# Kernel optimization log

Hardware: AMD Instinct MI355X
Metric: run time of the kernel (lower is better)

Reference implementation:

```python
import jax, jax.numpy as jnp
import numpy as np

B, N, E = 4, 50000, 800000
C_IN, C_OUT, OUT = 64, 64, 32


def _uniform(key, shape, fan_in):
    s = 1.0 / np.sqrt(fan_in)
    return jax.random.uniform(key, shape, jnp.float32, -s, s)


def setup_inputs() -> dict:
    key = jax.random.key(0)
    ks = jax.random.split(key, 16)
    x = jax.random.normal(ks[0], (B, N, C_IN), jnp.float32)
    edge_index = jax.random.randint(ks[1], (2, E), 0, N, jnp.int64)
    edge_weight = jax.random.uniform(ks[2], (E,), jnp.float32)
    # GCNConv weights (in->out) and biases for z, r, h gates
    Wz = _uniform(ks[3], (C_IN, C_OUT), C_IN); bz = jnp.zeros((C_OUT,), jnp.float32)
    Wr = _uniform(ks[4], (C_IN, C_OUT), C_IN); br = jnp.zeros((C_OUT,), jnp.float32)
    Wh = _uniform(ks[5], (C_IN, C_OUT), C_IN); bh = jnp.zeros((C_OUT,), jnp.float32)
    # gating Linears: (2*out -> out)
    Lz = _uniform(ks[6], (2 * C_OUT, C_OUT), 2 * C_OUT); Lzb = _uniform(ks[7], (C_OUT,), 2 * C_OUT)
    Lr = _uniform(ks[8], (2 * C_OUT, C_OUT), 2 * C_OUT); Lrb = _uniform(ks[9], (C_OUT,), 2 * C_OUT)
    Lh = _uniform(ks[10], (2 * C_OUT, C_OUT), 2 * C_OUT); Lhb = _uniform(ks[11], (C_OUT,), 2 * C_OUT)
    # output head Linear(out_channels -> out_size)
    Hw = _uniform(ks[12], (C_OUT, OUT), C_OUT); Hb = _uniform(ks[13], (OUT,), C_OUT)
    return dict(x=x, edge_index=edge_index, edge_weight=edge_weight,
                Wz=Wz, bz=bz, Wr=Wr, br=br, Wh=Wh, bh=bh,
                Lz=Lz, Lzb=Lzb, Lr=Lr, Lrb=Lrb, Lh=Lh, Lhb=Lhb,
                Hw=Hw, Hb=Hb)


def _gcn(x, W, b, src, tgt, norm):
    # x: (B, N, Cin) -> (B, N, Cout); sym-normalized aggregation over edges
    xw = jnp.einsum('bnf,fo->bno', x, W)
    msg = xw[:, src] * norm[None, :, None]          # (B, E+N, Cout)
    agg = jnp.zeros_like(xw).at[:, tgt].add(msg)    # scatter-add at targets
    return agg + b


def reference(x, edge_index, edge_weight, Wz, bz, Wr, br, Wh, bh,
              Lz, Lzb, Lr, Lrb, Lh, Lhb, Hw, Hb):
    src, tgt = edge_index[0], edge_index[1]
    loop = jnp.arange(N)
    src_f = jnp.concatenate([src, loop])
    tgt_f = jnp.concatenate([tgt, loop])
    w_f = jnp.concatenate([edge_weight, jnp.ones((N,), edge_weight.dtype)])
    deg = jnp.zeros((N,), w_f.dtype).at[tgt_f].add(w_f)  # self-loops => deg >= 1
    dinv = jax.lax.rsqrt(deg)
    norm = dinv[src_f] * w_f * dinv[tgt_f]
    H = jnp.zeros((x.shape[0], N, Wz.shape[1]), x.dtype)  # TGCN2 initial hidden state
    gz = _gcn(x, Wz, bz, src_f, tgt_f, norm)
    Z = jax.nn.sigmoid(jnp.concatenate([gz, H], -1) @ Lz + Lzb)
    gr = _gcn(x, Wr, br, src_f, tgt_f, norm)
    R = jax.nn.sigmoid(jnp.concatenate([gr, H], -1) @ Lr + Lrb)
    gh = _gcn(x, Wh, bh, src_f, tgt_f, norm)
    Ht = jnp.tanh(jnp.concatenate([gh, H * R], -1) @ Lh + Lhb)
    Hn = Z * H + (1.0 - Z) * Ht
    return jax.nn.relu(Hn) @ Hw + Hb
```

## Files before the change

### kernel.cpp

```cpp
#include <hip/hip_runtime.h>
#include <stdint.h>

#define N_NODES 50000
#define N_EDGES 800000
#define XSTRIDE 3200000
#define PS      3200000
#define PSU     1600000
#define EBLK    3125
#define XPBLK   12500
#define MAXDEG  64
#define CSH     24
#define WMASK   0xFFFFFFu

typedef __attribute__((ext_vector_type(8))) short short8;
typedef __attribute__((ext_vector_type(4))) float float4v;

static __device__ __forceinline__ unsigned f2bf(float f) {
  unsigned u = __float_as_uint(f);
  return (u + 0x7fffu + ((u >> 16) & 1u)) >> 16;
}
static __device__ __forceinline__ float bflo(unsigned u) { return __uint_as_float(u << 16); }
static __device__ __forceinline__ float bfhi(unsigned u) { return __uint_as_float(u & 0xffff0000u); }

__global__ __launch_bounds__(256) void k_atomic_frag(
    const int* __restrict__ tgt, const int* __restrict__ src,
    const float* __restrict__ ew,
    unsigned* __restrict__ packed32, int2* __restrict__ colw,
    const float* __restrict__ Wz, const float* __restrict__ bz,
    const float* __restrict__ Wh, const float* __restrict__ bh,
    const float* __restrict__ Lz, const float* __restrict__ Lzb,
    const float* __restrict__ Lh, const float* __restrict__ Lhb,
    const float* __restrict__ Hw,
    ushort* __restrict__ BG, ushort* __restrict__ BH, float* __restrict__ czh) {
  int blk = blockIdx.x;
  if (blk < EBLK) {
    int e = blk * 256 + threadIdx.x;
    int t = tgt[e], s = src[e];
    t = t < 0 ? 0 : (t >= N_NODES ? N_NODES - 1 : t);
    s = s < 0 ? 0 : (s >= N_NODES ? N_NODES - 1 : s);
    float wv = ew[e];
    wv = wv < 0.f ? 0.f : wv;
    unsigned fix = (unsigned)(wv * 262144.0f);
    fix = fix > 262143u ? 262143u : fix;
    unsigned old = atomicAdd(&packed32[t], (1u << CSH) | fix);
    unsigned rank = old >> CSH;
    if (rank < MAXDEG)
      colw[t * MAXDEG + (int)rank] = make_int2(s, __float_as_int(wv));
    return;
  }
  int idx = (blk - EBLK) * 256 + threadIdx.x;
  if (idx < 16384) {
    int i = idx & 7, lane = (idx >> 3) & 63, kk = (idx >> 9) & 1;
    int jt = (idx >> 10) & 7, hilo = idx >> 13;
    int c = kk * 32 + ((lane >> 4) << 3) + i;
    int jj0 = jt * 16 + (lane & 15);
    const float* W = (jj0 < 64) ? Wz : Wh;
    const float* L = (jj0 < 64) ? Lz : Lh;
    int jj = jj0 & 63;
    float v = 0.f;
    #pragma unroll 8
    for (int k = 0; k < 64; ++k) v += W[c * 64 + k] * L[k * 64 + jj];
    unsigned hi = f2bf(v);
    BG[idx] = hilo ? (ushort)f2bf(v - bflo(hi)) : (ushort)hi;
  } else if (idx < 20480) {
    int t = idx - 16384;
    int i = t & 7, lane = (t >> 3) & 63, kk = (t >> 9) & 1;
    int ot = (t >> 10) & 1, hilo = (t >> 11) & 1;
    int c = kk * 32 + ((lane >> 4) << 3) + i;
    int o = ot * 16 + (lane & 15);
    float v = Hw[c * 32 + o];
    unsigned hi = f2bf(v);
    BH[t] = hilo ? (ushort)f2bf(v - bflo(hi)) : (ushort)hi;
  } else if (idx < 20608) {
    int jj0 = idx - 20480;
    int jj = jj0 & 63;
    const float* L  = (jj0 < 64) ? Lz  : Lh;
    const float* bb = (jj0 < 64) ? bz  : bh;
    const float* Lb = (jj0 < 64) ? Lzb : Lhb;
    float v = Lb[jj];
    #pragma unroll 8
    for (int k = 0; k < 64; ++k) v += bb[k] * L[k * 64 + jj];
    czh[jj0] = v;
  }
}

__global__ __launch_bounds__(256) void k_xpose(
    const float* __restrict__ x, const unsigned* __restrict__ packed32,
    uint2* __restrict__ xp) {
  int i = blockIdx.x * 256 + threadIdx.x;
  int n = i >> 6;
  unsigned pk = packed32[n];
  float dinv = rsqrtf(1.0f + (float)(pk & WMASK) * 0x1p-18f);
  float v0 = x[i] * dinv;
  float v1 = x[i + XSTRIDE] * dinv;
  float v2 = x[i + 2 * XSTRIDE] * dinv;
  float v3 = x[i + 3 * XSTRIDE] * dinv;
  uint2 u;
  u.x = (f2bf(v1) << 16) | f2bf(v0);
  u.y = (f2bf(v3) << 16) | f2bf(v2);
  xp[i] = u;
}

__global__ __launch_bounds__(256) void kagg(
    const uint4* __restrict__ xp4, const unsigned* __restrict__ packed32,
    const int4* __restrict__ colw4, unsigned* __restrict__ aggp32) {
  int lane = threadIdx.x & 63;
  int w = threadIdx.x >> 6;
  int n = blockIdx.x * 4 + w;
  int c2 = lane & 31;
  int eh = lane >> 5;
  unsigned pk = packed32[n];
  int cnt = (int)(pk >> CSH);
  cnt = cnt > MAXDEG ? MAXDEG : cnt;
  float dinv_n = rsqrtf(1.0f + (float)(pk & WMASK) * 0x1p-18f);
  float a0, a1, a2, a3, b0, b1, b2, b3;
  {
    float g = eh ? 0.0f : 1.0f;
    uint4 q = xp4[(size_t)n * 32 + c2];
    a0 = g * bflo(q.x); a1 = g * bfhi(q.x);
    a2 = g * bflo(q.y); a3 = g * bfhi(q.y);
    b0 = g * bflo(q.z); b1 = g * bfhi(q.z);
    b2 = g * bflo(q.w); b3 = g * bfhi(q.w);
  }
  const int4* row = colw4 + (size_t)n * (MAXDEG / 2);
  const int2* row2 = (const int2*)row;
  int p = 0;
  for (; p + 8 <= cnt; p += 8) {
    int4 m0 = row[(p >> 1) + 2 * eh];
    int4 m1 = row[(p >> 1) + 2 * eh + 1];
    float w0 = __int_as_float(m0.y), w1 = __int_as_float(m0.w);
    float w2 = __int_as_float(m1.y), w3 = __int_as_float(m1.w);
    uint4 q0 = xp4[(size_t)m0.x * 32 + c2];
    uint4 q1 = xp4[(size_t)m0.z * 32 + c2];
    uint4 q2 = xp4[(size_t)m1.x * 32 + c2];
    uint4 q3 = xp4[(size_t)m1.z * 32 + c2];
    a0 += w0*bflo(q0.x) + w1*bflo(q1.x) + w2*bflo(q2.x) + w3*bflo(q3.x);
    a1 += w0*bfhi(q0.x) + w1*bfhi(q1.x) + w2*bfhi(q2.x) + w3*bfhi(q3.x);
    a2 += w0*bflo(q0.y) + w1*bflo(q1.y) + w2*bflo(q2.y) + w3*bflo(q3.y);
    a3 += w0*bfhi(q0.y) + w1*bfhi(q1.y) + w2*bfhi(q2.y) + w3*bfhi(q3.y);
    b0 += w0*bflo(q0.z) + w1*bflo(q1.z) + w2*bflo(q2.z) + w3*bflo(q3.z);
    b1 += w0*bfhi(q0.z) + w1*bfhi(q1.z) + w2*bfhi(q2.z) + w3*bfhi(q3.z);
    b2 += w0*bflo(q0.w) + w1*bflo(q1.w) + w2*bflo(q2.w) + w3*bflo(q3.w);
    b3 += w0*bfhi(q0.w) + w1*bfhi(q1.w) + w2*bfhi(q2.w) + w3*bfhi(q3.w);
  }
  for (; p + 2 <= cnt; p += 2) {
    int2 m = row2[p + eh];
    float wv = __int_as_float(m.y);
    uint4 q = xp4[(size_t)m.x * 32 + c2];
    a0 += wv * bflo(q.x); a1 += wv * bfhi(q.x);
    a2 += wv * bflo(q.y); a3 += wv * bfhi(q.y);
    b0 += wv * bflo(q.z); b1 += wv * bfhi(q.z);
    b2 += wv * bflo(q.w); b3 += wv * bfhi(q.w);
  }
  if (p < cnt) {
    int2 m = row2[p];
    float wv = eh ? 0.0f : __int_as_float(m.y);
    uint4 q = xp4[(size_t)m.x * 32 + c2];
    a0 += wv * bflo(q.x); a1 += wv * bfhi(q.x);
    a2 += wv * bflo(q.y); a3 += wv * bfhi(q.y);
    b0 += wv * bflo(q.z); b1 += wv * bfhi(q.z);
    b2 += wv * bflo(q.w); b3 += wv * bfhi(q.w);
  }
  a0 += __shfl_xor(a0, 32, 64); a1 += __shfl_xor(a1, 32, 64);
  a2 += __shfl_xor(a2, 32, 64); a3 += __shfl_xor(a3, 32, 64);
  b0 += __shfl_xor(b0, 32, 64); b1 += __shfl_xor(b1, 32, 64);
  b2 += __shfl_xor(b2, 32, 64); b3 += __shfl_xor(b3, 32, 64);
  float pa = dinv_n * (eh ? a2 : a0), pb = dinv_n * (eh ? b2 : b0);
  float qa = dinv_n * (eh ? a3 : a1), qb = dinv_n * (eh ? b3 : b1);
  unsigned vlo = f2bf(pa) | (f2bf(pb) << 16);
  unsigned vhi = f2bf(qa) | (f2bf(qb) << 16);
  size_t base = (size_t)(eh * 2) * PSU + (size_t)n * 32 + c2;
  aggp32[base]       = vlo;
  aggp32[base + PSU] = vhi;
}

__global__ __launch_bounds__(256) void kdense(
    const ushort* __restrict__ aggp,
    const ushort* __restrict__ BG, const ushort* __restrict__ BH,
    const float* __restrict__ czh, const float* __restrict__ Hb,
    float* __restrict__ out) {
  __shared__ uint4 sBGv[2048];
  __shared__ uint4 sBHv[512];
  __shared__ float sCzh[128];
  __shared__ float sHb[32];
  __shared__ uint4 sRv[4][128];

  int tid = threadIdx.x;
  {
    const uint4* g = (const uint4*)BG;
    for (int i = tid; i < 2048; i += 256) sBGv[i] = g[i];
    const uint4* g2 = (const uint4*)BH;
    for (int i = tid; i < 512; i += 256) sBHv[i] = g2[i];
    if (tid < 128) sCzh[tid] = czh[tid];
    if (tid < 32) sHb[tid] = Hb[tid];
  }
  __syncthreads();

  int lane = tid & 63;
  int w = tid >> 6;
  int tile = blockIdx.x * 4 + w;
  int b = tile / 3125;
  int n0 = (tile - b * 3125) * 16;

  const ushort* ap = aggp + (size_t)b * PS + (size_t)(n0 + (lane & 15)) * 64
                     + ((lane >> 4) << 3);
  short8 a0 = *(const short8*)(ap);
  short8 a1 = *(const short8*)(ap + 32);

  float4v acc[8];
  #pragma unroll
  for (int jt = 0; jt < 8; ++jt) {
    float bias = sCzh[jt * 16 + (lane & 15)];
    acc[jt] = (float4v){bias, bias, bias, bias};
  }
  const short8* bgf = (const short8*)sBGv;
  #pragma unroll
  for (int hilo = 0; hilo < 2; ++hilo) {
    #pragma unroll
    for (int jt = 0; jt < 8; ++jt) {
      short8 b0 = bgf[((hilo * 8 + jt) * 2 + 0) * 64 + lane];
      short8 b1 = bgf[((hilo * 8 + jt) * 2 + 1) * 64 + lane];
      acc[jt] = __builtin_amdgcn_mfma_f32_16x16x32_bf16(a0, b0, acc[jt], 0, 0, 0);
      acc[jt] = __builtin_amdgcn_mfma_f32_16x16x32_bf16(a1, b1, acc[jt], 0, 0, 0);
    }
  }

  char* rbase = (char*)(&sRv[w][0]);
  int rowg = (lane >> 4) * 4;
  int colb = lane & 15;
  #pragma unroll
  for (int jt = 0; jt < 4; ++jt) {
    #pragma unroll
    for (int r = 0; r < 4; ++r) {
      float z = acc[jt][r], h = acc[jt + 4][r];
      float s = 1.f / (1.f + __expf(-z));
      float e = __expf(2.f * h);
      float t = (e - 1.f) / (e + 1.f);
      float rr = (1.f - s) * t;
      rr = rr > 0.f ? rr : 0.f;
      int row = rowg + r;
      int colx = jt * 16 + colb;
      int byte = (row * 128 + colx * 2) ^ ((row & 7) << 4);
      *(ushort*)(rbase + byte) = (ushort)f2bf(rr);
    }
  }
  __syncthreads();

  short8 ra0, ra1;
  {
    int row = lane & 15;
    int g = (lane >> 4) << 4;
    int swz = (row & 7) << 4;
    ra0 = *(const short8*)(rbase + row * 128 + ((g) ^ swz));
    ra1 = *(const short8*)(rbase + row * 128 + ((64 + g) ^ swz));
  }
  float4v hacc[2];
  #pragma unroll
  for (int ot = 0; ot < 2; ++ot) {
    float hb = sHb[ot * 16 + (lane & 15)];
    hacc[ot] = (float4v){hb, hb, hb, hb};
  }
  const short8* bhf = (const short8*)sBHv;
  #pragma unroll
  for (int hilo = 0; hilo < 2; ++hilo) {
    #pragma unroll
    for (int ot = 0; ot < 2; ++ot) {
      short8 b0 = bhf[((hilo * 2 + ot) * 2 + 0) * 64 + lane];
      short8 b1 = bhf[((hilo * 2 + ot) * 2 + 1) * 64 + lane];
      hacc[ot] = __builtin_amdgcn_mfma_f32_16x16x32_bf16(ra0, b0, hacc[ot], 0, 0, 0);
      hacc[ot] = __builtin_amdgcn_mfma_f32_16x16x32_bf16(ra1, b1, hacc[ot], 0, 0, 0);
    }
  }
  float* ob = out + ((size_t)b * N_NODES + n0) * 32;
  #pragma unroll
  for (int ot = 0; ot < 2; ++ot) {
    #pragma unroll
    for (int r = 0; r < 4; ++r) {
      int row = rowg + r;
      int o = ot * 16 + (lane & 15);
      ob[row * 32 + o] = hacc[ot][r];
    }
  }
}

extern "C" void kernel_launch(void* const* d_in, const int* in_sizes, int n_in,
                              void* d_out, int out_size, void* d_ws, size_t ws_size,
                              hipStream_t stream) {
  const float* x   = (const float*)d_in[0];
  const int*   ei  = (const int*)d_in[1];
  const float* ew  = (const float*)d_in[2];
  const float* Wz  = (const float*)d_in[3];
  const float* bz  = (const float*)d_in[4];
  const float* Wh  = (const float*)d_in[7];
  const float* bh  = (const float*)d_in[8];
  const float* Lz  = (const float*)d_in[9];
  const float* Lzb = (const float*)d_in[10];
  const float* Lh  = (const float*)d_in[13];
  const float* Lhb = (const float*)d_in[14];
  const float* Hw  = (const float*)d_in[15];
  const float* Hb  = (const float*)d_in[16];
  float* out = (float*)d_out;

  const int* src = ei;
  const int* tgt = ei + N_EDGES;

  char* ws = (char*)d_ws;
  ws = (char*)(((uintptr_t)ws + 255) & ~(uintptr_t)255);
  unsigned* packed32 = (unsigned*)ws; ws += (size_t)N_NODES * 4;
  ws = (char*)(((uintptr_t)ws + 255) & ~(uintptr_t)255);
  int2* colw = (int2*)ws;      ws += (size_t)N_NODES * MAXDEG * 8;
  ushort* BG    = (ushort*)ws; ws += 16384 * 2;
  ushort* BH    = (ushort*)ws; ws += 4096 * 2;
  float* czh    = (float*)ws;  ws += 128 * 4;
  ws = (char*)(((uintptr_t)ws + 255) & ~(uintptr_t)255);
  uint2* xp     = (uint2*)ws;  ws += (size_t)N_NODES * 64 * 8;
  unsigned* aggp32 = (unsigned*)ws; ws += (size_t)4 * PSU * 4;

  hipMemsetAsync(packed32, 0, (size_t)N_NODES * 4, stream);
  k_atomic_frag<<<EBLK + 81, 256, 0, stream>>>(
      tgt, src, ew, packed32, colw,
      Wz, bz, Wh, bh, Lz, Lzb, Lh, Lhb, Hw, BG, BH, czh);
  k_xpose<<<XPBLK, 256, 0, stream>>>(x, packed32, xp);
  kagg<<<N_NODES / 4, 256, 0, stream>>>((const uint4*)xp, packed32,
                                        (const int4*)colw, aggp32);
  kdense<<<3125, 256, 0, stream>>>((const ushort*)aggp32, BG, BH, czh, Hb, out);
}
```

Baseline: 151.6 us.

## Fuse edge bucketing with x transpose, move source dinv into aggregation

Stops scaling x by the source node's dinv during the transpose. The transpose can then run inside the same launch as the edge atomic bucketing and weight prep, with edge blocks interleaved one in five. In exchange, the aggregation kernel gathers packed32 for every neighbor to apply the source dinv, which adds random 4-byte loads per edge. The dense kernel is made persistent at 625 blocks, each looping over 5 tiles to reuse the shared-memory weight loads, at the cost of an extra barrier per tile.

```diff
diff --git a/kernel.cpp b/kernel.cpp
--- a/kernel.cpp
+++ b/kernel.cpp
@@ -8,6 +8,7 @@
 #define PSU     1600000
 #define EBLK    3125
 #define XPBLK   12500
+#define FUSE_T  15730
 #define MAXDEG  64
 #define CSH     24
 #define WMASK   0xFFFFFFu
@@ -21,8 +22,12 @@
 }
 static __device__ __forceinline__ float bflo(unsigned u) { return __uint_as_float(u << 16); }
 static __device__ __forceinline__ float bfhi(unsigned u) { return __uint_as_float(u & 0xffff0000u); }
-
-__global__ __launch_bounds__(256) void k_atomic_frag(
+static __device__ __forceinline__ float dinv_of(unsigned pk) {
+  return rsqrtf(1.0f + (float)(pk & WMASK) * 0x1p-18f);
+}
+
+__global__ __launch_bounds__(256) void kfused(
+    const float* __restrict__ x, uint2* __restrict__ xp,
     const int* __restrict__ tgt, const int* __restrict__ src,
     const float* __restrict__ ew,
     unsigned* __restrict__ packed32, int2* __restrict__ colw,
@@ -33,8 +38,10 @@
     const float* __restrict__ Hw,
     ushort* __restrict__ BG, ushort* __restrict__ BH, float* __restrict__ czh) {
   int blk = blockIdx.x;
-  if (blk < EBLK) {
-    int e = blk * 256 + threadIdx.x;
+  if (blk % 5 == 0) {
+    int eb = blk / 5;
+    if (eb >= EBLK) return;
+    int e = eb * 256 + threadIdx.x;
     int t = tgt[e], s = src[e];
     t = t < 0 ? 0 : (t >= N_NODES ? N_NODES - 1 : t);
     s = s < 0 ? 0 : (s >= N_NODES ? N_NODES - 1 : s);
@@ -48,7 +55,20 @@
       colw[t * MAXDEG + (int)rank] = make_int2(s, __float_as_int(wv));
     return;
   }
-  int idx = (blk - EBLK) * 256 + threadIdx.x;
+  int j = blk - blk / 5 - 1;
+  if (j < XPBLK) {
+    int i = j * 256 + threadIdx.x;
+    float v0 = x[i];
+    float v1 = x[i + XSTRIDE];
+    float v2 = x[i + 2 * XSTRIDE];
+    float v3 = x[i + 3 * XSTRIDE];
+    uint2 u;
+    u.x = (f2bf(v1) << 16) | f2bf(v0);
+    u.y = (f2bf(v3) << 16) | f2bf(v2);
+    xp[i] = u;
+    return;
+  }
+  int idx = (j - XPBLK) * 256 + threadIdx.x;
   if (idx < 16384) {
     int i = idx & 7, lane = (idx >> 3) & 63, kk = (idx >> 9) & 1;
     int jt = (idx >> 10) & 7, hilo = idx >> 13;
@@ -84,23 +104,6 @@
   }
 }
 
-__global__ __launch_bounds__(256) void k_xpose(
-    const float* __restrict__ x, const unsigned* __restrict__ packed32,
-    uint2* __restrict__ xp) {
-  int i = blockIdx.x * 256 + threadIdx.x;
-  int n = i >> 6;
-  unsigned pk = packed32[n];
-  float dinv = rsqrtf(1.0f + (float)(pk & WMASK) * 0x1p-18f);
-  float v0 = x[i] * dinv;
-  float v1 = x[i + XSTRIDE] * dinv;
-  float v2 = x[i + 2 * XSTRIDE] * dinv;
-  float v3 = x[i + 3 * XSTRIDE] * dinv;
-  uint2 u;
-  u.x = (f2bf(v1) << 16) | f2bf(v0);
-  u.y = (f2bf(v3) << 16) | f2bf(v2);
-  xp[i] = u;
-}
-
 __global__ __launch_bounds__(256) void kagg(
     const uint4* __restrict__ xp4, const unsigned* __restrict__ packed32,
     const int4* __restrict__ colw4, unsigned* __restrict__ aggp32) {
@@ -112,10 +115,10 @@
   unsigned pk = packed32[n];
   int cnt = (int)(pk >> CSH);
   cnt = cnt > MAXDEG ? MAXDEG : cnt;
-  float dinv_n = rsqrtf(1.0f + (float)(pk & WMASK) * 0x1p-18f);
+  float dinv_n = dinv_of(pk);
   float a0, a1, a2, a3, b0, b1, b2, b3;
   {
-    float g = eh ? 0.0f : 1.0f;
+    float g = eh ? 0.0f : dinv_n;
     uint4 q = xp4[(size_t)n * 32 + c2];
     a0 = g * bflo(q.x); a1 = g * bfhi(q.x);
     a2 = g * bflo(q.y); a3 = g * bfhi(q.y);
@@ -128,8 +131,10 @@
   for (; p + 8 <= cnt; p += 8) {
     int4 m0 = row[(p >> 1) + 2 * eh];
     int4 m1 = row[(p >> 1) + 2 * eh + 1];
-    float w0 = __int_as_float(m0.y), w1 = __int_as_float(m0.w);
-    float w2 = __int_as_float(m1.y), w3 = __int_as_float(m1.w);
+    float w0 = __int_as_float(m0.y) * dinv_of(packed32[m0.x]);
+    float w1 = __int_as_float(m0.w) * dinv_of(packed32[m0.z]);
+    float w2 = __int_as_float(m1.y) * dinv_of(packed32[m1.x]);
+    float w3 = __int_as_float(m1.w) * dinv_of(packed32[m1.z]);
     uint4 q0 = xp4[(size_t)m0.x * 32 + c2];
     uint4 q1 = xp4[(size_t)m0.z * 32 + c2];
     uint4 q2 = xp4[(size_t)m1.x * 32 + c2];
@@ -145,7 +150,7 @@
   }
   for (; p + 2 <= cnt; p += 2) {
     int2 m = row2[p + eh];
-    float wv = __int_as_float(m.y);
+    float wv = __int_as_float(m.y) * dinv_of(packed32[m.x]);
     uint4 q = xp4[(size_t)m.x * 32 + c2];
     a0 += wv * bflo(q.x); a1 += wv * bfhi(q.x);
     a2 += wv * bflo(q.y); a3 += wv * bfhi(q.y);
@@ -154,7 +159,7 @@
   }
   if (p < cnt) {
     int2 m = row2[p];
-    float wv = eh ? 0.0f : __int_as_float(m.y);
+    float wv = eh ? 0.0f : __int_as_float(m.y) * dinv_of(packed32[m.x]);
     uint4 q = xp4[(size_t)m.x * 32 + c2];
     a0 += wv * bflo(q.x); a1 += wv * bfhi(q.x);
     a2 += wv * bflo(q.y); a3 += wv * bfhi(q.y);
@@ -198,88 +203,93 @@
 
   int lane = tid & 63;
   int w = tid >> 6;
-  int tile = blockIdx.x * 4 + w;
-  int b = tile / 3125;
-  int n0 = (tile - b * 3125) * 16;
-
-  const ushort* ap = aggp + (size_t)b * PS + (size_t)(n0 + (lane & 15)) * 64
-                     + ((lane >> 4) << 3);
-  short8 a0 = *(const short8*)(ap);
-  short8 a1 = *(const short8*)(ap + 32);
-
-  float4v acc[8];
-  #pragma unroll
-  for (int jt = 0; jt < 8; ++jt) {
-    float bias = sCzh[jt * 16 + (lane & 15)];
-    acc[jt] = (float4v){bias, bias, bias, bias};
-  }
   const short8* bgf = (const short8*)sBGv;
-  #pragma unroll
-  for (int hilo = 0; hilo < 2; ++hilo) {
-    #pragma unroll
-    for (int jt = 0; jt < 8; ++jt) {
-      short8 b0 = bgf[((hilo * 8 + jt) * 2 + 0) * 64 + lane];
-      short8 b1 = bgf[((hilo * 8 + jt) * 2 + 1) * 64 + lane];
-      acc[jt] = __builtin_amdgcn_mfma_f32_16x16x32_bf16(a0, b0, acc[jt], 0, 0, 0);
-      acc[jt] = __builtin_amdgcn_mfma_f32_16x16x32_bf16(a1, b1, acc[jt], 0, 0, 0);
-    }
-  }
-
+  const short8* bhf = (const short8*)sBHv;
   char* rbase = (char*)(&sRv[w][0]);
   int rowg = (lane >> 4) * 4;
   int colb = lane & 15;
-  #pragma unroll
-  for (int jt = 0; jt < 4; ++jt) {
-    #pragma unroll
-    for (int r = 0; r < 4; ++r) {
-      float z = acc[jt][r], h = acc[jt + 4][r];
-      float s = 1.f / (1.f + __expf(-z));
-      float e = __expf(2.f * h);
-      float t = (e - 1.f) / (e + 1.f);
-      float rr = (1.f - s) * t;
-      rr = rr > 0.f ? rr : 0.f;
-      int row = rowg + r;
-      int colx = jt * 16 + colb;
-      int byte = (row * 128 + colx * 2) ^ ((row & 7) << 4);
-      *(ushort*)(rbase + byte) = (ushort)f2bf(rr);
-    }
-  }
-  __syncthreads();
-
-  short8 ra0, ra1;
-  {
-    int row = lane & 15;
-    int g = (lane >> 4) << 4;
-    int swz = (row & 7) << 4;
-    ra0 = *(const short8*)(rbase + row * 128 + ((g) ^ swz));
-    ra1 = *(const short8*)(rbase + row * 128 + ((64 + g) ^ swz));
-  }
-  float4v hacc[2];
-  #pragma unroll
-  for (int ot = 0; ot < 2; ++ot) {
-    float hb = sHb[ot * 16 + (lane & 15)];
-    hacc[ot] = (float4v){hb, hb, hb, hb};
-  }
-  const short8* bhf = (const short8*)sBHv;
-  #pragma unroll
-  for (int hilo = 0; hilo < 2; ++hilo) {
+
+  #pragma unroll 1
+  for (int it = 0; it < 5; ++it) {
+    int tile = (it * 625 + blockIdx.x) * 4 + w;
+    int b = tile / 3125;
+    int n0 = (tile - b * 3125) * 16;
+
+    const ushort* ap = aggp + (size_t)b * PS + (size_t)(n0 + (lane & 15)) * 64
+                       + ((lane >> 4) << 3);
+    short8 a0 = *(const short8*)(ap);
+    short8 a1 = *(const short8*)(ap + 32);
+
+    float4v acc[8];
+    #pragma unroll
+    for (int jt = 0; jt < 8; ++jt) {
+      float bias = sCzh[jt * 16 + (lane & 15)];
+      acc[jt] = (float4v){bias, bias, bias, bias};
+    }
+    #pragma unroll
+    for (int hilo = 0; hilo < 2; ++hilo) {
+      #pragma unroll
+      for (int jt = 0; jt < 8; ++jt) {
+        short8 b0 = bgf[((hilo * 8 + jt) * 2 + 0) * 64 + lane];
+        short8 b1 = bgf[((hilo * 8 + jt) * 2 + 1) * 64 + lane];
+        acc[jt] = __builtin_amdgcn_mfma_f32_16x16x32_bf16(a0, b0, acc[jt], 0, 0, 0);
+        acc[jt] = __builtin_amdgcn_mfma_f32_16x16x32_bf16(a1, b1, acc[jt], 0, 0, 0);
+      }
+    }
+
+    #pragma unroll
+    for (int jt = 0; jt < 4; ++jt) {
+      #pragma unroll
+      for (int r = 0; r < 4; ++r) {
+        float z = acc[jt][r], h = acc[jt + 4][r];
+        float s = 1.f / (1.f + __expf(-z));
+        float e = __expf(2.f * h);
+        float t = (e - 1.f) / (e + 1.f);
+        float rr = (1.f - s) * t;
+        rr = rr > 0.f ? rr : 0.f;
+        int row = rowg + r;
+        int colx = jt * 16 + colb;
+        int byte = (row * 128 + colx * 2) ^ ((row & 7) << 4);
+        *(ushort*)(rbase + byte) = (ushort)f2bf(rr);
+      }
+    }
+    __syncthreads();
+
+    short8 ra0, ra1;
+    {
+      int row = lane & 15;
+      int g = (lane >> 4) << 4;
+      int swz = (row & 7) << 4;
+      ra0 = *(const short8*)(rbase + row * 128 + ((g) ^ swz));
+      ra1 = *(const short8*)(rbase + row * 128 + ((64 + g) ^ swz));
+    }
+    float4v hacc[2];
     #pragma unroll
     for (int ot = 0; ot < 2; ++ot) {
-      short8 b0 = bhf[((hilo * 2 + ot) * 2 + 0) * 64 + lane];
-      short8 b1 = bhf[((hilo * 2 + ot) * 2 + 1) * 64 + lane];
-      hacc[ot] = __builtin_amdgcn_mfma_f32_16x16x32_bf16(ra0, b0, hacc[ot], 0, 0, 0);
-      hacc[ot] = __builtin_amdgcn_mfma_f32_16x16x32_bf16(ra1, b1, hacc[ot], 0, 0, 0);
-    }
-  }
-  float* ob = out + ((size_t)b * N_NODES + n0) * 32;
-  #pragma unroll
-  for (int ot = 0; ot < 2; ++ot) {
-    #pragma unroll
-    for (int r = 0; r < 4; ++r) {
-      int row = rowg + r;
-      int o = ot * 16 + (lane & 15);
-      ob[row * 32 + o] = hacc[ot][r];
-    }
+      float hb = sHb[ot * 16 + (lane & 15)];
+      hacc[ot] = (float4v){hb, hb, hb, hb};
+    }
+    #pragma unroll
+    for (int hilo = 0; hilo < 2; ++hilo) {
+      #pragma unroll
+      for (int ot = 0; ot < 2; ++ot) {
+        short8 b0 = bhf[((hilo * 2 + ot) * 2 + 0) * 64 + lane];
+        short8 b1 = bhf[((hilo * 2 + ot) * 2 + 1) * 64 + lane];
+        hacc[ot] = __builtin_amdgcn_mfma_f32_16x16x32_bf16(ra0, b0, hacc[ot], 0, 0, 0);
+        hacc[ot] = __builtin_amdgcn_mfma_f32_16x16x32_bf16(ra1, b1, hacc[ot], 0, 0, 0);
+      }
+    }
+    float* ob = out + ((size_t)b * N_NODES + n0) * 32;
+    #pragma unroll
+    for (int ot = 0; ot < 2; ++ot) {
+      #pragma unroll
+      for (int r = 0; r < 4; ++r) {
+        int row = rowg + r;
+        int o = ot * 16 + (lane & 15);
+        ob[row * 32 + o] = hacc[ot][r];
+      }
+    }
+    __syncthreads();
   }
 }
 
@@ -317,11 +327,10 @@
   unsigned* aggp32 = (unsigned*)ws; ws += (size_t)4 * PSU * 4;
 
   hipMemsetAsync(packed32, 0, (size_t)N_NODES * 4, stream);
-  k_atomic_frag<<<EBLK + 81, 256, 0, stream>>>(
-      tgt, src, ew, packed32, colw,
+  kfused<<<FUSE_T, 256, 0, stream>>>(
+      x, xp, tgt, src, ew, packed32, colw,
       Wz, bz, Wh, bh, Lz, Lzb, Lh, Lhb, Hw, BG, BH, czh);
-  k_xpose<<<XPBLK, 256, 0, stream>>>(x, packed32, xp);
   kagg<<<N_NODES / 4, 256, 0, stream>>>((const uint4*)xp, packed32,
                                         (const int4*)colw, aggp32);
-  kdense<<<3125, 256, 0, stream>>>((const ushort*)aggp32, BG, BH, czh, Hb, out);
-}
+  kdense<<<625, 256, 0, stream>>>((const ushort*)aggp32, BG, BH, czh, Hb, out);
+}
```

Result: faster. 144.5 us (-4.7%).
